# Kernel optimization log

Measured on AMD Instinct MI355X. Metric: run time of the kernel, lower is better.

## Reference

```python
import jax, jax.numpy as jnp
import numpy as np

V = 54  # len(nonterminals)
D = 512  # term_embedding_dim
LEAVES = 60000
LEVELS = 10


def _structure():
    rng = np.random.default_rng(0)
    sizes = [LEAVES]
    for _ in range(LEVELS - 1):
        sizes.append(sizes[-1] // 2)
    starts = np.concatenate([[0], np.cumsum(sizes)]).astype(np.int64)
    N = int(starts[-1])
    node_types = rng.integers(0, V, N).astype(np.int32)
    edge_child, edge_parent, edge_starts = [], [], [0, 0]
    for l in range(1, LEVELS):
        n_l = sizes[l]
        c1 = rng.integers(starts[l - 1], starts[l], n_l)  # child at height l-1 (defines height)
        c2 = rng.integers(0, starts[l], n_l)              # second child anywhere below
        edge_child.append(np.stack([c1, c2], 1).ravel())
        edge_parent.append(np.repeat(np.arange(n_l), 2))
        edge_starts.append(edge_starts[-1] + 2 * n_l)
    edge_child = np.concatenate(edge_child).astype(np.int64)
    edge_parent = np.concatenate(edge_parent).astype(np.int64)
    edge_starts = np.asarray(edge_starts, dtype=np.int64)
    roots = np.arange(starts[-2], starts[-1], dtype=np.int64)  # top-level nodes
    return node_types, starts, edge_child, edge_parent, edge_starts, roots


def setup_inputs() -> dict:
    node_types, level_starts, edge_child, edge_parent_local, edge_level_starts, roots = _structure()
    key = jax.random.key(0)
    ks = jax.random.split(key, 9)
    k = 1.0 / np.sqrt(D)
    u = lambda kk, shape: jax.random.uniform(kk, shape, jnp.float32, -k, k)
    return {
        "node_types": jnp.asarray(node_types),
        "level_starts": level_starts,
        "edge_child": jnp.asarray(edge_child),
        "edge_parent_local": jnp.asarray(edge_parent_local),
        "edge_level_starts": edge_level_starts,
        "roots": jnp.asarray(roots),
        "W_if": u(ks[0], (D, V)),
        "W_hf": u(ks[1], (D, D)),
        "b_f": u(ks[2], (D,)),
        "W_i": u(ks[3], (D, V + D)),
        "b_i": u(ks[4], (D,)),
        "W_o": u(ks[5], (D, V + D)),
        "b_o": u(ks[6], (D,)),
        "W_u": u(ks[7], (D, V + D)),
        "b_u": u(ks[8], (D,)),
    }


def reference(node_types, level_starts, edge_child, edge_parent_local, edge_level_starts,
              roots, W_if, W_hf, b_f, W_i, b_i, W_o, b_o, W_u, b_u):
    ls = np.asarray(level_starts)
    es = np.asarray(edge_level_starts)
    N = int(ls[-1])
    dt = W_if.dtype
    H = jnp.zeros((N, D), dtype=dt)
    C = jnp.zeros((N, D), dtype=dt)
    for l in range(len(ls) - 1):
        s, e = int(ls[l]), int(ls[l + 1])
        n = e - s
        x = jax.nn.one_hot(node_types[s:e], V, dtype=dt)  # [n, V]
        if l == 0:
            h_sum = jnp.zeros((n, D), dtype=dt)
            c_remain = jnp.zeros((n, D), dtype=dt)
        else:
            a, b = int(es[l]), int(es[l + 1])
            ci = edge_child[a:b]
            pj = edge_parent_local[a:b]
            h_ch = H[ci]  # [e_l, D] gather of children hidden states
            c_ch = C[ci]
            h_sum = jax.ops.segment_sum(h_ch, pj, num_segments=n)
            Wx = x @ W_if.T  # [n, D]
            f = jax.nn.sigmoid(Wx[pj] + h_ch @ W_hf.T + b_f)  # per-edge forget gates
            c_remain = jax.ops.segment_sum(f * c_ch, pj, num_segments=n)
        xh = jnp.concatenate([x, h_sum], axis=1)  # [n, V+D]
        i_g = jax.nn.sigmoid(xh @ W_i.T + b_i)
        o_g = jax.nn.sigmoid(xh @ W_o.T + b_o)
        u = jnp.tanh(xh @ W_u.T + b_u)
        cells = i_g * u + c_remain
        hid = o_g * jnp.tanh(cells)
        H = H.at[s:e].set(hid)
        C = C.at[s:e].set(cells)
    return H[roots]
```

## Files before the change

kernel.cpp:

```cpp
#include <hip/hip_runtime.h>
#include <hip/hip_bf16.h>

#define DD 512
#define VV 54
#define NLEAF 60000
#define NINT 59881

typedef __attribute__((ext_vector_type(8))) short bf16x8;
typedef __attribute__((ext_vector_type(4))) float f32x4;

__device__ __forceinline__ float bflo(unsigned int u) {
    union { unsigned int i; float f; } v; v.i = u << 16; return v.f;
}
__device__ __forceinline__ float bfhi(unsigned int u) {
    union { unsigned int i; float f; } v; v.i = u & 0xffff0000u; return v.f;
}
__device__ __forceinline__ float bfu2f(unsigned short u) {
    union { unsigned int i; float f; } v; v.i = ((unsigned int)u) << 16; return v.f;
}
__device__ __forceinline__ unsigned short f2bfu(float f) {
    union { unsigned int i; float f; } v; v.f = f;
    unsigned int x = v.i;
    return (unsigned short)((x + 0x7FFFu + ((x >> 16) & 1u)) >> 16);
}
__device__ __forceinline__ unsigned int pack2(float lo, float hi) {
    return (unsigned int)f2bfu(lo) | ((unsigned int)f2bfu(hi) << 16);
}
__device__ __forceinline__ float b2f(__hip_bfloat16 x) { return __bfloat162float(x); }
__device__ __forceinline__ float sigm(float x) { return 1.f / (1.f + __expf(-x)); }

__device__ __forceinline__ void ld8(const __hip_bfloat16* p, float* o) {
    uint4 v = *(const uint4*)p;
    const unsigned short* s = (const unsigned short*)&v;
#pragma unroll
    for (int j = 0; j < 8; j++) o[j] = bfu2f(s[j]);
}
__device__ __forceinline__ void ldf8(const float* p, float* o) {
    float4 a = *(const float4*)p, b = *(const float4*)(p + 4);
    o[0] = a.x; o[1] = a.y; o[2] = a.z; o[3] = a.w;
    o[4] = b.x; o[5] = b.y; o[6] = b.z; o[7] = b.w;
}

__global__ void detect_idx64(const int* __restrict__ ec, int* __restrict__ flag) {
    __shared__ int nz;
    if (threadIdx.x == 0) nz = 0;
    __syncthreads();
    if (ec[2 * threadIdx.x + 1] != 0) atomicAdd(&nz, 1);
    __syncthreads();
    if (threadIdx.x == 0) flag[0] = (nz == 0) ? 1 : 0;
}

__global__ void prep_tables(const float* __restrict__ W_if, const float* __restrict__ b_f,
                            const float* __restrict__ W_i, const float* __restrict__ b_i,
                            const float* __restrict__ W_o, const float* __restrict__ b_o,
                            const float* __restrict__ W_u, const float* __restrict__ b_u,
                            float* __restrict__ wifc, float* __restrict__ tbi,
                            float* __restrict__ tbo, float* __restrict__ tbu,
                            __hip_bfloat16* __restrict__ hleaf, __hip_bfloat16* __restrict__ cleaf) {
    int t = blockIdx.x;
    for (int d = threadIdx.x; d < DD; d += blockDim.x) {
        wifc[t * DD + d] = W_if[d * VV + t] + b_f[d];
        float vi = W_i[d * (VV + DD) + t] + b_i[d];
        float vo = W_o[d * (VV + DD) + t] + b_o[d];
        float vu = W_u[d * (VV + DD) + t] + b_u[d];
        tbi[t * DD + d] = vi; tbo[t * DD + d] = vo; tbu[t * DD + d] = vu;
        float gi = sigm(vi), go = sigm(vo), gu = tanhf(vu);
        float c = gi * gu;
        float h = go * tanhf(c);
        hleaf[t * DD + d] = __float2bfloat16(h);
        cleaf[t * DD + d] = __float2bfloat16(c);
    }
}

__global__ void prep_wall(const float* __restrict__ W_hf, const float* __restrict__ W_i,
                          const float* __restrict__ W_o, const float* __restrict__ W_u,
                          __hip_bfloat16* __restrict__ Wall) {
    int idx = blockIdx.x * 256 + threadIdx.x;
    int m = idx >> 18;
    int rem = idx & (DD * DD - 1);
    float v;
    if (m == 0) {
        v = W_hf[rem];
    } else {
        int d = rem >> 9, k = rem & 511;
        const float* W = (m == 1) ? W_i : ((m == 2) ? W_o : W_u);
        v = W[d * (VV + DD) + VV + k];
    }
    Wall[idx] = __float2bfloat16(v);
}

__global__ void prep_pleaf(const __hip_bfloat16* __restrict__ hleaf,
                           const __hip_bfloat16* __restrict__ Wall,
                           __hip_bfloat16* __restrict__ Pleaf) {
    __shared__ float hsh[DD];
    int tt = blockIdx.x;
    int cb = blockIdx.y;
    for (int k = threadIdx.x; k < DD; k += 256) hsh[k] = b2f(hleaf[tt * DD + k]);
    __syncthreads();
    int c = cb * 256 + threadIdx.x;
    const __hip_bfloat16* wrow = Wall + (size_t)c * DD;
    float s = 0.f;
#pragma unroll 4
    for (int kq = 0; kq < 64; kq++) {
        uint4 v = *(const uint4*)(wrow + kq * 8);
        const unsigned short* vs = (const unsigned short*)&v;
#pragma unroll
        for (int e = 0; e < 8; e++) s += bfu2f(vs[e]) * hsh[kq * 8 + e];
    }
    Pleaf[(size_t)tt * 2048 + c] = __float2bfloat16(s);
}

__device__ __forceinline__ const __hip_bfloat16* h_row(int ci,
        const __hip_bfloat16* __restrict__ Hint, const __hip_bfloat16* __restrict__ hleaf,
        const int* __restrict__ nt) {
    return (ci < NLEAF) ? (hleaf + (size_t)nt[ci] * DD) : (Hint + (size_t)(ci - NLEAF) * DD);
}
__device__ __forceinline__ const __hip_bfloat16* c_row(int ci,
        const __hip_bfloat16* __restrict__ Cint, const __hip_bfloat16* __restrict__ cleaf,
        const int* __restrict__ nt) {
    return (ci < NLEAF) ? (cleaf + (size_t)nt[ci] * DD) : (Cint + (size_t)(ci - NLEAF) * DD);
}

__global__ __launch_bounds__(256) void gather_cell(
    const __hip_bfloat16* __restrict__ Pleaf,
    const __hip_bfloat16* __restrict__ cleaf,
    const int* __restrict__ nt, const int* __restrict__ ecb, int eoff,
    const int* __restrict__ ntl, const float* __restrict__ wifc,
    const float* __restrict__ tbi, const float* __restrict__ tbo,
    const float* __restrict__ tbu,
    __hip_bfloat16* __restrict__ Hout, __hip_bfloat16* __restrict__ Cout,
    const int* __restrict__ idx64, int n) {
    int idx = blockIdx.x * 256 + threadIdx.x;
    int p = idx >> 6;
    if (p >= n) return;
    const int mode = idx64[0];
    const int d0 = (idx & 63) << 3;
    int c1 = ecb[(eoff + 2 * p) << mode];
    int c2 = ecb[(eoff + 2 * p + 1) << mode];
    int t1 = nt[c1], t2 = nt[c2];
    int tp = ntl[p];
    const __hip_bfloat16* P1 = Pleaf + (size_t)t1 * 2048;
    const __hip_bfloat16* P2 = Pleaf + (size_t)t2 * 2048;
    float f1[8], f2v[8], i1[8], i2[8], o1[8], o2[8], u1[8], u2[8], x1[8], x2[8];
    ld8(P1 + d0, f1);         ld8(P2 + d0, f2v);
    ld8(P1 + 512 + d0, i1);   ld8(P2 + 512 + d0, i2);
    ld8(P1 + 1024 + d0, o1);  ld8(P2 + 1024 + d0, o2);
    ld8(P1 + 1536 + d0, u1);  ld8(P2 + 1536 + d0, u2);
    ld8(cleaf + (size_t)t1 * DD + d0, x1);
    ld8(cleaf + (size_t)t2 * DD + d0, x2);
    float wf[8], vb[8], ob[8], ub[8];
    ldf8(wifc + (size_t)tp * DD + d0, wf);
    ldf8(tbi + (size_t)tp * DD + d0, vb);
    ldf8(tbo + (size_t)tp * DD + d0, ob);
    ldf8(tbu + (size_t)tp * DD + d0, ub);
    float hv[8], cv[8];
#pragma unroll
    for (int j = 0; j < 8; j++) {
        float fr = sigm(f1[j] + wf[j]) * x1[j] + sigm(f2v[j] + wf[j]) * x2[j];
        float gi = sigm(i1[j] + i2[j] + vb[j]);
        float go = sigm(o1[j] + o2[j] + ob[j]);
        float gu = tanhf(u1[j] + u2[j] + ub[j]);
        float c = gi * gu + fr;
        cv[j] = c;
        hv[j] = go * tanhf(c);
    }
    uint4 hp, cp;
    hp.x = pack2(hv[0], hv[1]); hp.y = pack2(hv[2], hv[3]);
    hp.z = pack2(hv[4], hv[5]); hp.w = pack2(hv[6], hv[7]);
    cp.x = pack2(cv[0], cv[1]); cp.y = pack2(cv[2], cv[3]);
    cp.z = pack2(cv[4], cv[5]); cp.w = pack2(cv[6], cv[7]);
    *(uint4*)(Hout + (size_t)p * DD + d0) = hp;
    *(uint4*)(Cout + (size_t)p * DD + d0) = cp;
}

__device__ __forceinline__ void mm_f_step(const char* buf, int wr, int wc, int lane,
                                          f32x4 (&acc)[4][4]) {
    bf16x8 af[4], bfr[4];
#pragma unroll
    for (int i = 0; i < 4; i++)
        af[i] = *(const bf16x8*)(buf + (wr * 4 + i) * 1024 + lane * 16);
#pragma unroll
    for (int j = 0; j < 4; j++)
        bfr[j] = *(const bf16x8*)(buf + 8192 + (wc * 4 + j) * 1024 + lane * 16);
#pragma unroll
    for (int i = 0; i < 4; i++)
#pragma unroll
        for (int j = 0; j < 4; j++)
            acc[i][j] = __builtin_amdgcn_mfma_f32_16x16x32_bf16(af[i], bfr[j], acc[i][j], 0, 0, 0);
}

__device__ __forceinline__ void mm_g_step(const char* lds, int wr, int wc, int lane,
                                          f32x4 (&acc)[3][2][2]) {
    bf16x8 af[2];
#pragma unroll
    for (int i = 0; i < 2; i++)
        af[i] = *(const bf16x8*)(lds + (wr * 2 + i) * 1024 + lane * 16);
#pragma unroll
    for (int g = 0; g < 3; g++)
#pragma unroll
        for (int j = 0; j < 2; j++) {
            bf16x8 bg = *(const bf16x8*)(lds + 4096 + g * 4096 + (wc * 2 + j) * 1024 + lane * 16);
#pragma unroll
            for (int i = 0; i < 2; i++)
                acc[g][i][j] = __builtin_amdgcn_mfma_f32_16x16x32_bf16(af[i], bg, acc[g][i][j], 0, 0, 0);
        }
}

__device__ __forceinline__ void mm_fu_step(const char* buf, int wr, int wc, int lane,
                                           f32x4 (&acc)[4][2][2]) {
    bf16x8 af[2];
#pragma unroll
    for (int i = 0; i < 2; i++)
        af[i] = *(const bf16x8*)(buf + (wr * 2 + i) * 1024 + lane * 16);
#pragma unroll
    for (int m = 0; m < 4; m++) {
        bf16x8 b0 = *(const bf16x8*)(buf + 4096 + m * 4096 + (wc * 2 + 0) * 1024 + lane * 16);
        bf16x8 b1 = *(const bf16x8*)(buf + 4096 + m * 4096 + (wc * 2 + 1) * 1024 + lane * 16);
        acc[m][0][0] = __builtin_amdgcn_mfma_f32_16x16x32_bf16(af[0], b0, acc[m][0][0], 0, 0, 0);
        acc[m][0][1] = __builtin_amdgcn_mfma_f32_16x16x32_bf16(af[0], b1, acc[m][0][1], 0, 0, 0);
        acc[m][1][0] = __builtin_amdgcn_mfma_f32_16x16x32_bf16(af[1], b0, acc[m][1][0], 0, 0, 0);
        acc[m][1][1] = __builtin_amdgcn_mfma_f32_16x16x32_bf16(af[1], b1, acc[m][1][1], 0, 0, 0);
    }
}

__global__ __launch_bounds__(256) void gemm_f(
    const __hip_bfloat16* __restrict__ Hint, const __hip_bfloat16* __restrict__ Cint,
    const __hip_bfloat16* __restrict__ hleaf, const __hip_bfloat16* __restrict__ cleaf,
    const int* __restrict__ nt, const __hip_bfloat16* __restrict__ Wall,
    const int* __restrict__ ecb, int eoff, const int* __restrict__ ntl,
    const float* __restrict__ wifc, __hip_bfloat16* __restrict__ crem,
    const int* __restrict__ idx64, int n) {
    __shared__ char lds[32768];
    const int M = 2 * n;
    const int R = (M + 127) >> 7;
    const int id = blockIdx.x, xcd = id & 7, q = id >> 3;
    const int rt = xcd + ((q >> 2) << 3), ct = q & 3;
    if (rt >= R) return;
    const int mode = idx64[0];
    const int t = threadIdx.x;
    const int lane = t & 63, w = t >> 6, wr = w >> 1, wc = w & 1;
    const int row0 = rt * 128, col0 = ct * 128;

    const int srow = t & 127;
    const int sc = t >> 7;
    const __hip_bfloat16* aptr = nullptr;
    {
        int e = row0 + srow;
        if (e < M) aptr = h_row(ecb[(eoff + e) << mode], Hint, hleaf, nt);
    }
    const __hip_bfloat16* bptr = Wall + (size_t)(col0 + srow) * DD;
    const int wb = (srow >> 4) * 1024 + (srow & 15) * 16;

    f32x4 acc[4][4];
#pragma unroll
    for (int i = 0; i < 4; i++)
#pragma unroll
        for (int j = 0; j < 4; j++) acc[i][j] = {0.f, 0.f, 0.f, 0.f};

    uint4 raE0 = {0,0,0,0}, raE1 = {0,0,0,0}, raO0 = {0,0,0,0}, raO1 = {0,0,0,0};
    uint4 rb0, rb1;
    if (aptr) {
        raE0 = *(const uint4*)(aptr + sc * 8);
        raE1 = *(const uint4*)(aptr + (sc + 2) * 8);
        raO0 = *(const uint4*)(aptr + 32 + sc * 8);
        raO1 = *(const uint4*)(aptr + 32 + (sc + 2) * 8);
    }
    rb0 = *(const uint4*)(bptr + sc * 8);
    rb1 = *(const uint4*)(bptr + (sc + 2) * 8);

#pragma unroll 1
    for (int kt = 0; kt < 16; kt += 2) {
        {
            char* buf = lds;
            *(uint4*)(buf + wb + sc * 256) = raE0;
            *(uint4*)(buf + wb + (sc + 2) * 256) = raE1;
            *(uint4*)(buf + 8192 + wb + sc * 256) = rb0;
            *(uint4*)(buf + 8192 + wb + (sc + 2) * 256) = rb1;
            __syncthreads();
            if (kt < 14 && aptr) {
                int ko = (kt + 2) * 32;
                raE0 = *(const uint4*)(aptr + ko + sc * 8);
                raE1 = *(const uint4*)(aptr + ko + (sc + 2) * 8);
            }
            {
                int ko = (kt + 1) * 32;
                rb0 = *(const uint4*)(bptr + ko + sc * 8);
                rb1 = *(const uint4*)(bptr + ko + (sc + 2) * 8);
            }
            mm_f_step(buf, wr, wc, lane, acc);
        }
        {
            char* buf = lds + 16384;
            *(uint4*)(buf + wb + sc * 256) = raO0;
            *(uint4*)(buf + wb + (sc + 2) * 256) = raO1;
            *(uint4*)(buf + 8192 + wb + sc * 256) = rb0;
            *(uint4*)(buf + 8192 + wb + (sc + 2) * 256) = rb1;
            __syncthreads();
            if (kt < 13 && aptr) {
                int ko = (kt + 3) * 32;
                raO0 = *(const uint4*)(aptr + ko + sc * 8);
                raO1 = *(const uint4*)(aptr + ko + (sc + 2) * 8);
            }
            if (kt < 14) {
                int ko = (kt + 2) * 32;
                rb0 = *(const uint4*)(bptr + ko + sc * 8);
                rb1 = *(const uint4*)(bptr + ko + (sc + 2) * 8);
            }
            mm_f_step(buf, wr, wc, lane, acc);
        }
    }

    __hip_bfloat16* ldsCr = (__hip_bfloat16*)lds;
    __syncthreads();
    const int colb = wc * 64;
#pragma unroll
    for (int i = 0; i < 4; i++) {
        int er0l = wr * 64 + i * 16 + ((lane >> 4) << 2);
        int er0 = row0 + er0l;
        if (er0 >= M) continue;
        bool hi = (er0 + 2) < M;
        int p0 = er0 >> 1;
        int p0l = er0l >> 1;
        int t0 = ntl[p0];
        int t1 = hi ? ntl[p0 + 1] : 0;
        int ci0 = ecb[(eoff + er0) << mode];
        int ci1 = ecb[(eoff + er0 + 1) << mode];
        int ci2 = hi ? ecb[(eoff + er0 + 2) << mode] : ci0;
        int ci3 = hi ? ecb[(eoff + er0 + 3) << mode] : ci0;
        const __hip_bfloat16* cp0 = c_row(ci0, Cint, cleaf, nt);
        const __hip_bfloat16* cp1 = c_row(ci1, Cint, cleaf, nt);
        const __hip_bfloat16* cp2 = c_row(ci2, Cint, cleaf, nt);
        const __hip_bfloat16* cp3 = c_row(ci3, Cint, cleaf, nt);
        const float* wfa = wifc + (size_t)t0 * DD;
        const float* wfb = wifc + (size_t)t1 * DD;
#pragma unroll
        for (int j = 0; j < 4; j++) {
            int coll = colb + j * 16 + (lane & 15);
            int col = col0 + coll;
            float wa = wfa[col], wbv = wfb[col];
            float s0 = sigm(acc[i][j].x + wa) * b2f(cp0[col])
                     + sigm(acc[i][j].y + wa) * b2f(cp1[col]);
            ldsCr[p0l * 128 + coll] = __float2bfloat16(s0);
            if (hi) {
                float s1 = sigm(acc[i][j].z + wbv) * b2f(cp2[col])
                         + sigm(acc[i][j].w + wbv) * b2f(cp3[col]);
                ldsCr[(p0l + 1) * 128 + coll] = __float2bfloat16(s1);
            }
        }
    }
    __syncthreads();
    {
        int prow = t >> 2, seg = t & 3;
        int p = (row0 >> 1) + prow;
        if (p < n) {
            const uint4* src = (const uint4*)(lds + prow * 256 + seg * 64);
            uint4* dst = (uint4*)(crem + (size_t)p * DD + col0 + seg * 32);
            dst[0] = src[0]; dst[1] = src[1]; dst[2] = src[2]; dst[3] = src[3];
        }
    }
}

__global__ __launch_bounds__(256) void gemm_g2(
    const __hip_bfloat16* __restrict__ Hint, const __hip_bfloat16* __restrict__ hleaf,
    const int* __restrict__ nt, const __hip_bfloat16* __restrict__ Wall,
    const int* __restrict__ ecb, int eoff, const int* __restrict__ ntl,
    const float* __restrict__ tbi, const float* __restrict__ tbo,
    const float* __restrict__ tbu, const __hip_bfloat16* __restrict__ crem,
    __hip_bfloat16* __restrict__ Hrow, __hip_bfloat16* __restrict__ Crow,
    float* __restrict__ outF, const int* __restrict__ idx64, int n) {
    __shared__ char lds[16384];
    const int R = (n + 63) >> 6;
    const int id = blockIdx.x, xcd = id & 7, q = id >> 3;
    const int rt = xcd + ((q >> 3) << 3), ct = q & 7;
    if (rt >= R) return;
    const int mode = idx64[0];
    const int t = threadIdx.x;
    const int lane = t & 63, w = t >> 6, wr = w >> 1, wc = w & 1;
    const int row0 = rt * 64, col0 = ct * 64;

    const int arow = t & 63, achk = t >> 6;
    const __hip_bfloat16 *pa = nullptr, *pb = nullptr;
    {
        int p = row0 + arow;
        if (p < n) {
            int c0 = ecb[(eoff + 2 * p) << mode];
            int c1 = ecb[(eoff + 2 * p + 1) << mode];
            pa = h_row(c0, Hint, hleaf, nt) + achk * 8;
            pb = h_row(c1, Hint, hleaf, nt) + achk * 8;
        }
    }
    const int wrA = (arow >> 4) * 1024 + (arow & 15) * 16 + achk * 256;
    const __hip_bfloat16* bbase = Wall + (size_t)(512 + col0 + arow) * DD + achk * 8;
    const int wrB = 4096 + wrA;

    f32x4 acc[3][2][2];
#pragma unroll
    for (int g = 0; g < 3; g++)
#pragma unroll
        for (int i = 0; i < 2; i++)
#pragma unroll
            for (int j = 0; j < 2; j++) acc[g][i][j] = {0.f, 0.f, 0.f, 0.f};

    uint4 raxE = {0,0,0,0}, rayE = {0,0,0,0}, raxO = {0,0,0,0}, rayO = {0,0,0,0};
    uint4 rb[3];
    if (pa) {
        raxE = *(const uint4*)pa;        rayE = *(const uint4*)pb;
        raxO = *(const uint4*)(pa + 32); rayO = *(const uint4*)(pb + 32);
    }
#pragma unroll
    for (int g = 0; g < 3; g++) rb[g] = *(const uint4*)(bbase + (size_t)g * DD * DD);

#pragma unroll 1
    for (int kt = 0; kt < 16; kt += 2) {
        {
            uint4 av;
            av.x = pack2(bflo(raxE.x) + bflo(rayE.x), bfhi(raxE.x) + bfhi(rayE.x));
            av.y = pack2(bflo(raxE.y) + bflo(rayE.y), bfhi(raxE.y) + bfhi(rayE.y));
            av.z = pack2(bflo(raxE.z) + bflo(rayE.z), bfhi(raxE.z) + bfhi(rayE.z));
            av.w = pack2(bflo(raxE.w) + bflo(rayE.w), bfhi(raxE.w) + bfhi(rayE.w));
            *(uint4*)(lds + wrA) = av;
#pragma unroll
            for (int g = 0; g < 3; g++) *(uint4*)(lds + wrB + g * 4096) = rb[g];
            __syncthreads();
            if (kt < 14 && pa) {
                int ko = (kt + 2) * 32;
                raxE = *(const uint4*)(pa + ko);
                rayE = *(const uint4*)(pb + ko);
            }
            {
                int ko = (kt + 1) * 32;
#pragma unroll
                for (int g = 0; g < 3; g++) rb[g] = *(const uint4*)(bbase + (size_t)g * DD * DD + ko);
            }
            mm_g_step(lds, wr, wc, lane, acc);
            __syncthreads();
        }
        {
            uint4 av;
            av.x = pack2(bflo(raxO.x) + bflo(rayO.x), bfhi(raxO.x) + bfhi(rayO.x));
            av.y = pack2(bflo(raxO.y) + bflo(rayO.y), bfhi(raxO.y) + bfhi(rayO.y));
            av.z = pack2(bflo(raxO.z) + bflo(rayO.z), bfhi(raxO.z) + bfhi(rayO.z));
            av.w = pack2(bflo(raxO.w) + bflo(rayO.w), bfhi(raxO.w) + bfhi(rayO.w));
            *(uint4*)(lds + wrA) = av;
#pragma unroll
            for (int g = 0; g < 3; g++) *(uint4*)(lds + wrB + g * 4096) = rb[g];
            __syncthreads();
            if (kt < 13 && pa) {
                int ko = (kt + 3) * 32;
                raxO = *(const uint4*)(pa + ko);
                rayO = *(const uint4*)(pb + ko);
            }
            if (kt < 14) {
                int ko = (kt + 2) * 32;
#pragma unroll
                for (int g = 0; g < 3; g++) rb[g] = *(const uint4*)(bbase + (size_t)g * DD * DD + ko);
            }
            mm_g_step(lds, wr, wc, lane, acc);
            __syncthreads();
        }
    }

    __hip_bfloat16* ldsH = (__hip_bfloat16*)lds;
    __hip_bfloat16* ldsC = (__hip_bfloat16*)(lds + 8192);
#pragma unroll
    for (int i = 0; i < 2; i++)
#pragma unroll
        for (int j = 0; j < 2; j++) {
            int coll = (wc * 2 + j) * 16 + (lane & 15);
            int col = col0 + coll;
#pragma unroll
            for (int r = 0; r < 4; r++) {
                int pl = wr * 32 + i * 16 + ((lane >> 4) << 2) + r;
                int p = row0 + pl;
                if (p >= n) continue;
                int tp = ntl[p];
                float gi = sigm(acc[0][i][j][r] + tbi[(size_t)tp * DD + col]);
                float go = sigm(acc[1][i][j][r] + tbo[(size_t)tp * DD + col]);
                float gu = tanhf(acc[2][i][j][r] + tbu[(size_t)tp * DD + col]);
                float c = gi * gu + b2f(crem[(size_t)p * DD + col]);
                float h = go * tanhf(c);
                ldsH[pl * 64 + coll] = __float2bfloat16(h);
                ldsC[pl * 64 + coll] = __float2bfloat16(c);
                if (outF) outF[(size_t)p * DD + col] = h;
            }
        }
    __syncthreads();
    {
        int prow = t >> 2, seg = t & 3;
        int p = row0 + prow;
        if (p < n) {
            uint4 h0 = *(uint4*)(lds + prow * 128 + seg * 32);
            uint4 h1 = *(uint4*)(lds + prow * 128 + seg * 32 + 16);
            uint4 c0 = *(uint4*)(lds + 8192 + prow * 128 + seg * 32);
            uint4 c1 = *(uint4*)(lds + 8192 + prow * 128 + seg * 32 + 16);
            *(uint4*)(Hrow + (size_t)p * DD + col0 + seg * 16) = h0;
            *(uint4*)(Hrow + (size_t)p * DD + col0 + seg * 16 + 8) = h1;
            *(uint4*)(Crow + (size_t)p * DD + col0 + seg * 16) = c0;
            *(uint4*)(Crow + (size_t)p * DD + col0 + seg * 16 + 8) = c1;
        }
    }
}

__global__ __launch_bounds__(256) void fused_mfma(
    const __hip_bfloat16* __restrict__ Hint, const __hip_bfloat16* __restrict__ Cint,
    const __hip_bfloat16* __restrict__ hleaf, const __hip_bfloat16* __restrict__ cleaf,
    const int* __restrict__ nt, const __hip_bfloat16* __restrict__ Wall,
    const int* __restrict__ ecb, int eoff, const int* __restrict__ ntl,
    const float* __restrict__ wifc, const float* __restrict__ tbi,
    const float* __restrict__ tbo, const float* __restrict__ tbu,
    __hip_bfloat16* __restrict__ Hrow, __hip_bfloat16* __restrict__ Crow,
    float* __restrict__ outF, const int* __restrict__ idx64, int n) {
    __shared__ char lds[40960];
    const int M = 2 * n;
    const int R = (M + 63) >> 6;
    const int id = blockIdx.x, xcd = id & 7, q = id >> 3;
    const int rt = xcd + ((q >> 3) << 3), ct = q & 7;
    if (rt >= R) return;
    const int mode = idx64[0];
    const int t = threadIdx.x;
    const int lane = t & 63, w = t >> 6, wr = w >> 1, wc = w & 1;
    const int row0 = rt * 64;
    const int col0 = ct * 64;

    const int srow = t & 63, schk = t >> 6;
    const int soff = (srow >> 4) * 1024 + (srow & 15) * 16 + schk * 256;

    const __hip_bfloat16* aptr = nullptr;
    {
        int e = row0 + srow;
        if (e < M) aptr = h_row(ecb[(eoff + e) << mode], Hint, hleaf, nt);
    }
    const __hip_bfloat16* bptr = Wall + (size_t)(col0 + srow) * DD + schk * 8;

    f32x4 acc[4][2][2];
#pragma unroll
    for (int m = 0; m < 4; m++)
#pragma unroll
        for (int i = 0; i < 2; i++)
#pragma unroll
            for (int j = 0; j < 2; j++) acc[m][i][j] = {0.f, 0.f, 0.f, 0.f};

    uint4 raE = {0,0,0,0}, raO = {0,0,0,0};
    uint4 rb[4];
    if (aptr) {
        raE = *(const uint4*)(aptr + schk * 8);
        raO = *(const uint4*)(aptr + 32 + schk * 8);
    }
#pragma unroll
    for (int m = 0; m < 4; m++) rb[m] = *(const uint4*)(bptr + (size_t)m * DD * DD);

#pragma unroll 1
    for (int kt = 0; kt < 16; kt += 2) {
        {
            char* buf = lds;
            *(uint4*)(buf + soff) = raE;
#pragma unroll
            for (int m = 0; m < 4; m++)
                *(uint4*)(buf + 4096 + m * 4096 + soff) = rb[m];
            __syncthreads();
            if (kt < 14 && aptr)
                raE = *(const uint4*)(aptr + (kt + 2) * 32 + schk * 8);
            {
                int ko = (kt + 1) * 32;
#pragma unroll
                for (int m = 0; m < 4; m++)
                    rb[m] = *(const uint4*)(bptr + (size_t)m * DD * DD + ko);
            }
            mm_fu_step(buf, wr, wc, lane, acc);
        }
        {
            char* buf = lds + 20480;
            *(uint4*)(buf + soff) = raO;
#pragma unroll
            for (int m = 0; m < 4; m++)
                *(uint4*)(buf + 4096 + m * 4096 + soff) = rb[m];
            __syncthreads();
            if (kt < 13 && aptr)
                raO = *(const uint4*)(aptr + (kt + 3) * 32 + schk * 8);
            if (kt < 14) {
                int ko = (kt + 2) * 32;
#pragma unroll
                for (int m = 0; m < 4; m++)
                    rb[m] = *(const uint4*)(bptr + (size_t)m * DD * DD + ko);
            }
            mm_fu_step(buf, wr, wc, lane, acc);
        }
    }

    __hip_bfloat16* ldsH = (__hip_bfloat16*)lds;
    __hip_bfloat16* ldsC = (__hip_bfloat16*)(lds + 4096);
    __syncthreads();

#pragma unroll
    for (int i = 0; i < 2; i++) {
        int er0l = wr * 32 + i * 16 + ((lane >> 4) << 2);
        int er0 = row0 + er0l;
        if (er0 >= M) continue;
        bool hi = (er0 + 2) < M;
        int p0 = er0 >> 1;
        int p0l = er0l >> 1;
        int tp0 = ntl[p0];
        int tp1 = hi ? ntl[p0 + 1] : 0;
        int ci0 = ecb[(eoff + er0) << mode];
        int ci1 = ecb[(eoff + er0 + 1) << mode];
        int ci2 = hi ? ecb[(eoff + er0 + 2) << mode] : ci0;
        int ci3 = hi ? ecb[(eoff + er0 + 3) << mode] : ci0;
        const __hip_bfloat16* cp0 = c_row(ci0, Cint, cleaf, nt);
        const __hip_bfloat16* cp1 = c_row(ci1, Cint, cleaf, nt);
        const __hip_bfloat16* cp2 = c_row(ci2, Cint, cleaf, nt);
        const __hip_bfloat16* cp3 = c_row(ci3, Cint, cleaf, nt);
#pragma unroll
        for (int j = 0; j < 2; j++) {
            int coll = (wc * 2 + j) * 16 + (lane & 15);
            int col = col0 + coll;
            f32x4 aF = acc[0][i][j], aI = acc[1][i][j], aO = acc[2][i][j], aU = acc[3][i][j];
            {
                float wf = wifc[(size_t)tp0 * DD + col];
                float fr = sigm(aF.x + wf) * b2f(cp0[col]) + sigm(aF.y + wf) * b2f(cp1[col]);
                float gi = sigm(aI.x + aI.y + tbi[(size_t)tp0 * DD + col]);
                float go = sigm(aO.x + aO.y + tbo[(size_t)tp0 * DD + col]);
                float gu = tanhf(aU.x + aU.y + tbu[(size_t)tp0 * DD + col]);
                float c = gi * gu + fr;
                float h = go * tanhf(c);
                ldsH[p0l * 64 + coll] = __float2bfloat16(h);
                ldsC[p0l * 64 + coll] = __float2bfloat16(c);
            }
            if (hi) {
                float wf = wifc[(size_t)tp1 * DD + col];
                float fr = sigm(aF.z + wf) * b2f(cp2[col]) + sigm(aF.w + wf) * b2f(cp3[col]);
                float gi = sigm(aI.z + aI.w + tbi[(size_t)tp1 * DD + col]);
                float go = sigm(aO.z + aO.w + tbo[(size_t)tp1 * DD + col]);
                float gu = tanhf(aU.z + aU.w + tbu[(size_t)tp1 * DD + col]);
                float c = gi * gu + fr;
                float h = go * tanhf(c);
                ldsH[(p0l + 1) * 64 + coll] = __float2bfloat16(h);
                ldsC[(p0l + 1) * 64 + coll] = __float2bfloat16(c);
            }
        }
    }
    __syncthreads();

    {
        int prow = t >> 3, seg = t & 7;
        int p = (row0 >> 1) + prow;
        if (p < n) {
            uint4 hv = *(uint4*)(lds + prow * 128 + seg * 16);
            uint4 cv = *(uint4*)(lds + 4096 + prow * 128 + seg * 16);
            *(uint4*)(Hrow + (size_t)p * DD + col0 + seg * 8) = hv;
            *(uint4*)(Crow + (size_t)p * DD + col0 + seg * 8) = cv;
            if (outF) {
                const unsigned short* hs = (const unsigned short*)&hv;
                float4 o0, o1;
                o0.x = bfu2f(hs[0]); o0.y = bfu2f(hs[1]); o0.z = bfu2f(hs[2]); o0.w = bfu2f(hs[3]);
                o1.x = bfu2f(hs[4]); o1.y = bfu2f(hs[5]); o1.z = bfu2f(hs[6]); o1.w = bfu2f(hs[7]);
                *(float4*)(outF + (size_t)p * DD + col0 + seg * 8) = o0;
                *(float4*)(outF + (size_t)p * DD + col0 + seg * 8 + 4) = o1;
            }
        }
    }
}

extern "C" void kernel_launch(void* const* d_in, const int* in_sizes, int n_in,
                              void* d_out, int out_size, void* d_ws, size_t ws_size,
                              hipStream_t stream) {
    const int* node_types = (const int*)d_in[0];
    const int* edge_child = (const int*)d_in[2];
    const float* W_if = (const float*)d_in[6];
    const float* W_hf = (const float*)d_in[7];
    const float* b_f = (const float*)d_in[8];
    const float* W_i = (const float*)d_in[9];
    const float* b_i = (const float*)d_in[10];
    const float* W_o = (const float*)d_in[11];
    const float* b_o = (const float*)d_in[12];
    const float* W_u = (const float*)d_in[13];
    const float* b_u = (const float*)d_in[14];
    float* out = (float*)d_out;

    static const int ls[11] = {0, 60000, 90000, 105000, 112500, 116250,
                               118125, 119062, 119530, 119764, 119881};
    static const int es[11] = {0, 0, 60000, 90000, 105000, 112500,
                               116250, 118124, 119060, 119528, 119762};

    char* ws = (char*)d_ws;
    size_t off = 0;
    auto alloc = [&](size_t bytes) -> void* {
        void* p = ws + off;
        off += (bytes + 255) & ~(size_t)255;
        return p;
    };
    int* flag = (int*)alloc(256);
    __hip_bfloat16* Wall = (__hip_bfloat16*)alloc((size_t)4 * DD * DD * 2);
    float* wifc = (float*)alloc((size_t)VV * DD * 4);
    float* tbi = (float*)alloc((size_t)VV * DD * 4);
    float* tbo = (float*)alloc((size_t)VV * DD * 4);
    float* tbu = (float*)alloc((size_t)VV * DD * 4);
    __hip_bfloat16* hleaf = (__hip_bfloat16*)alloc((size_t)VV * DD * 2);
    __hip_bfloat16* cleaf = (__hip_bfloat16*)alloc((size_t)VV * DD * 2);
    __hip_bfloat16* Pleaf = (__hip_bfloat16*)alloc((size_t)VV * 2048 * 2);
    __hip_bfloat16* Hint = (__hip_bfloat16*)alloc((size_t)NINT * DD * 2);
    __hip_bfloat16* Cint = (__hip_bfloat16*)alloc((size_t)NINT * DD * 2);
    __hip_bfloat16* crem = (__hip_bfloat16*)alloc((size_t)15000 * DD * 2);
    (void)ws_size; (void)in_sizes; (void)n_in; (void)out_size;

    detect_idx64<<<1, 128, 0, stream>>>(edge_child, flag);
    prep_tables<<<54, 256, 0, stream>>>(W_if, b_f, W_i, b_i, W_o, b_o, W_u, b_u,
                                        wifc, tbi, tbo, tbu, hleaf, cleaf);
    prep_wall<<<(4 * DD * DD) / 256, 256, 0, stream>>>(W_hf, W_i, W_o, W_u, Wall);
    {
        dim3 g(VV, 8);
        prep_pleaf<<<g, 256, 0, stream>>>(hleaf, Wall, Pleaf);
    }

    {
        int n = ls[2] - ls[1];
        gather_cell<<<(n * 64 + 255) / 256, 256, 0, stream>>>(
            Pleaf, cleaf, node_types, edge_child, es[1], node_types + ls[1],
            wifc, tbi, tbo, tbu, Hint, Cint, flag, n);
    }

    {
        int l = 2, s = ls[l], n = ls[l + 1] - s;
        int Rf = (2 * n + 127) / 128;
        gemm_f<<<8 * ((Rf + 7) / 8) * 4, 256, 0, stream>>>(
            Hint, Cint, hleaf, cleaf, node_types, Wall,
            edge_child, es[l], node_types + s, wifc, crem, flag, n);
        int Rg = (n + 63) / 64;
        gemm_g2<<<8 * ((Rg + 7) / 8) * 8, 256, 0, stream>>>(
            Hint, hleaf, node_types, Wall,
            edge_child, es[l], node_types + s, tbi, tbo, tbu, crem,
            Hint + (size_t)(s - NLEAF) * DD, Cint + (size_t)(s - NLEAF) * DD,
            nullptr, flag, n);
    }

    for (int l = 3; l < 10; l++) {
        int s = ls[l];
        int n = ls[l + 1] - s;
        int M2 = 2 * n;
        int Rf = (M2 + 63) / 64;
        int grid = 8 * ((Rf + 7) / 8) * 8;
        fused_mfma<<<grid, 256, 0, stream>>>(Hint, Cint, hleaf, cleaf, node_types, Wall,
                                             edge_child, es[l], node_types + s,
                                             wifc, tbi, tbo, tbu,
                                             Hint + (size_t)(s - NLEAF) * DD,
                                             Cint + (size_t)(s - NLEAF) * DD,
                                             (l == 9) ? out : nullptr, flag, n);
    }
}
```

Before: 805.7 us.

## Load MFMA operands directly from global memory, bypassing LDS staging, in upper-level kernel

For levels 3-9 the fused kernel no longer stages the gathered H rows and weight tiles through double-buffered LDS with barriers. Each wave now loads its MFMA fragments straight from global memory into registers and software-prefetches the next A fragment. This removes the LDS store/load traffic and the per-step __syncthreads, and shrinks LDS use so more blocks fit per CU. The cost is redundant global/L2 reads of the weights across waves and less coalesced 16-byte loads, which matters little on small upper levels but could stall on latency.

```diff
diff --git a/kernel.cpp b/kernel.cpp
--- a/kernel.cpp
+++ b/kernel.cpp
@@ -206,23 +206,6 @@
         }
 }
 
-__device__ __forceinline__ void mm_fu_step(const char* buf, int wr, int wc, int lane,
-                                           f32x4 (&acc)[4][2][2]) {
-    bf16x8 af[2];
-#pragma unroll
-    for (int i = 0; i < 2; i++)
-        af[i] = *(const bf16x8*)(buf + (wr * 2 + i) * 1024 + lane * 16);
-#pragma unroll
-    for (int m = 0; m < 4; m++) {
-        bf16x8 b0 = *(const bf16x8*)(buf + 4096 + m * 4096 + (wc * 2 + 0) * 1024 + lane * 16);
-        bf16x8 b1 = *(const bf16x8*)(buf + 4096 + m * 4096 + (wc * 2 + 1) * 1024 + lane * 16);
-        acc[m][0][0] = __builtin_amdgcn_mfma_f32_16x16x32_bf16(af[0], b0, acc[m][0][0], 0, 0, 0);
-        acc[m][0][1] = __builtin_amdgcn_mfma_f32_16x16x32_bf16(af[0], b1, acc[m][0][1], 0, 0, 0);
-        acc[m][1][0] = __builtin_amdgcn_mfma_f32_16x16x32_bf16(af[1], b0, acc[m][1][0], 0, 0, 0);
-        acc[m][1][1] = __builtin_amdgcn_mfma_f32_16x16x32_bf16(af[1], b1, acc[m][1][1], 0, 0, 0);
-    }
-}
-
 __global__ __launch_bounds__(256) void gemm_f(
     const __hip_bfloat16* __restrict__ Hint, const __hip_bfloat16* __restrict__ Cint,
     const __hip_bfloat16* __restrict__ hleaf, const __hip_bfloat16* __restrict__ cleaf,
@@ -501,7 +484,7 @@
     }
 }
 
-__global__ __launch_bounds__(256) void fused_mfma(
+__global__ __launch_bounds__(256) void fused_direct(
     const __hip_bfloat16* __restrict__ Hint, const __hip_bfloat16* __restrict__ Cint,
     const __hip_bfloat16* __restrict__ hleaf, const __hip_bfloat16* __restrict__ cleaf,
     const int* __restrict__ nt, const __hip_bfloat16* __restrict__ Wall,
@@ -510,7 +493,7 @@
     const float* __restrict__ tbo, const float* __restrict__ tbu,
     __hip_bfloat16* __restrict__ Hrow, __hip_bfloat16* __restrict__ Crow,
     float* __restrict__ outF, const int* __restrict__ idx64, int n) {
-    __shared__ char lds[40960];
+    __shared__ char lds[8192];
     const int M = 2 * n;
     const int R = (M + 63) >> 6;
     const int id = blockIdx.x, xcd = id & 7, q = id >> 3;
@@ -522,15 +505,17 @@
     const int row0 = rt * 64;
     const int col0 = ct * 64;
 
-    const int srow = t & 63, schk = t >> 6;
-    const int soff = (srow >> 4) * 1024 + (srow & 15) * 16 + schk * 256;
-
-    const __hip_bfloat16* aptr = nullptr;
-    {
-        int e = row0 + srow;
-        if (e < M) aptr = h_row(ecb[(eoff + e) << mode], Hint, hleaf, nt);
-    }
-    const __hip_bfloat16* bptr = Wall + (size_t)(col0 + srow) * DD + schk * 8;
+    const int rl = lane & 15, kc = lane >> 4;
+    const __hip_bfloat16 *pa0, *pa1;
+    {
+        int e0 = row0 + wr * 32 + rl;
+        int e1 = e0 + 16;
+        int c0 = (e0 < M) ? ecb[(eoff + e0) << mode] : 0;
+        int c1 = (e1 < M) ? ecb[(eoff + e1) << mode] : 0;
+        pa0 = h_row(c0, Hint, hleaf, nt) + kc * 8;
+        pa1 = h_row(c1, Hint, hleaf, nt) + kc * 8;
+    }
+    const __hip_bfloat16* pb = Wall + (size_t)(col0 + wc * 32 + rl) * DD + kc * 8;
 
     f32x4 acc[4][2][2];
 #pragma unroll
@@ -540,56 +525,28 @@
 #pragma unroll
             for (int j = 0; j < 2; j++) acc[m][i][j] = {0.f, 0.f, 0.f, 0.f};
 
-    uint4 raE = {0,0,0,0}, raO = {0,0,0,0};
-    uint4 rb[4];
-    if (aptr) {
-        raE = *(const uint4*)(aptr + schk * 8);
-        raO = *(const uint4*)(aptr + 32 + schk * 8);
-    }
-#pragma unroll
-    for (int m = 0; m < 4; m++) rb[m] = *(const uint4*)(bptr + (size_t)m * DD * DD);
-
+    bf16x8 a0n = *(const bf16x8*)pa0;
+    bf16x8 a1n = *(const bf16x8*)pa1;
 #pragma unroll 1
-    for (int kt = 0; kt < 16; kt += 2) {
-        {
-            char* buf = lds;
-            *(uint4*)(buf + soff) = raE;
-#pragma unroll
-            for (int m = 0; m < 4; m++)
-                *(uint4*)(buf + 4096 + m * 4096 + soff) = rb[m];
-            __syncthreads();
-            if (kt < 14 && aptr)
-                raE = *(const uint4*)(aptr + (kt + 2) * 32 + schk * 8);
-            {
-                int ko = (kt + 1) * 32;
-#pragma unroll
-                for (int m = 0; m < 4; m++)
-                    rb[m] = *(const uint4*)(bptr + (size_t)m * DD * DD + ko);
-            }
-            mm_fu_step(buf, wr, wc, lane, acc);
-        }
-        {
-            char* buf = lds + 20480;
-            *(uint4*)(buf + soff) = raO;
-#pragma unroll
-            for (int m = 0; m < 4; m++)
-                *(uint4*)(buf + 4096 + m * 4096 + soff) = rb[m];
-            __syncthreads();
-            if (kt < 13 && aptr)
-                raO = *(const uint4*)(aptr + (kt + 3) * 32 + schk * 8);
-            if (kt < 14) {
-                int ko = (kt + 2) * 32;
-#pragma unroll
-                for (int m = 0; m < 4; m++)
-                    rb[m] = *(const uint4*)(bptr + (size_t)m * DD * DD + ko);
-            }
-            mm_fu_step(buf, wr, wc, lane, acc);
+    for (int kt = 0; kt < 16; ++kt) {
+        bf16x8 af0 = a0n, af1 = a1n;
+        if (kt < 15) {
+            a0n = *(const bf16x8*)(pa0 + (kt + 1) * 32);
+            a1n = *(const bf16x8*)(pa1 + (kt + 1) * 32);
+        }
+#pragma unroll
+        for (int m = 0; m < 4; m++) {
+            bf16x8 b0 = *(const bf16x8*)(pb + (size_t)m * DD * DD + kt * 32);
+            bf16x8 b1 = *(const bf16x8*)(pb + (size_t)m * DD * DD + 16 * DD + kt * 32);
+            acc[m][0][0] = __builtin_amdgcn_mfma_f32_16x16x32_bf16(af0, b0, acc[m][0][0], 0, 0, 0);
+            acc[m][0][1] = __builtin_amdgcn_mfma_f32_16x16x32_bf16(af0, b1, acc[m][0][1], 0, 0, 0);
+            acc[m][1][0] = __builtin_amdgcn_mfma_f32_16x16x32_bf16(af1, b0, acc[m][1][0], 0, 0, 0);
+            acc[m][1][1] = __builtin_amdgcn_mfma_f32_16x16x32_bf16(af1, b1, acc[m][1][1], 0, 0, 0);
         }
     }
 
     __hip_bfloat16* ldsH = (__hip_bfloat16*)lds;
     __hip_bfloat16* ldsC = (__hip_bfloat16*)(lds + 4096);
-    __syncthreads();
 
 #pragma unroll
     for (int i = 0; i < 2; i++) {
@@ -738,11 +695,11 @@
         int M2 = 2 * n;
         int Rf = (M2 + 63) / 64;
         int grid = 8 * ((Rf + 7) / 8) * 8;
-        fused_mfma<<<grid, 256, 0, stream>>>(Hint, Cint, hleaf, cleaf, node_types, Wall,
-                                             edge_child, es[l], node_types + s,
-                                             wifc, tbi, tbo, tbu,
-                                             Hint + (size_t)(s - NLEAF) * DD,
-                                             Cint + (size_t)(s - NLEAF) * DD,
-                                             (l == 9) ? out : nullptr, flag, n);
-    }
-}
+        fused_direct<<<grid, 256, 0, stream>>>(Hint, Cint, hleaf, cleaf, node_types, Wall,
+                                               edge_child, es[l], node_types + s,
+                                               wifc, tbi, tbo, tbu,
+                                               Hint + (size_t)(s - NLEAF) * DD,
+                                               Cint + (size_t)(s - NLEAF) * DD,
+                                               (l == 9) ? out : nullptr, flag, n);
+    }
+}
```

Measured after the change: 727.7 us. 1.11x faster.
